# Kernel optimization log

Hardware: AMD Instinct MI355X
Metric: run time of the kernel (lower is better)

Reference implementation:

```python
import jax, jax.numpy as jnp
import numpy as np

N_NODES = 50000
N_REL = 8
D_IN = 128
D_OUT = 128
N_EDGES = 800000


def setup_inputs() -> dict:
    key = jax.random.key(0)
    k = jax.random.split(key, 6)
    # Xavier-ish scales for the learned params
    w_scale = (6.0 / (D_IN + D_OUT)) ** 0.5
    X = jax.random.normal(k[0], (N_NODES, D_IN), dtype=jnp.float32)
    W = jax.random.uniform(k[1], (N_REL, D_IN, D_OUT), dtype=jnp.float32,
                           minval=-w_scale, maxval=w_scale)
    W0 = jax.random.uniform(k[2], (D_IN, D_OUT), dtype=jnp.float32,
                            minval=-w_scale, maxval=w_scale)
    inv_norm = jnp.ones((N_REL, N_NODES), dtype=jnp.float32)  # init'd to ones in torch
    # COO edge list encoding the stacked sparse adjacency tensor adj_tensor[r, dst, src]
    edge_src = jax.random.randint(k[3], (N_EDGES,), 0, N_NODES, dtype=jnp.int32)
    edge_dst = jax.random.randint(k[4], (N_EDGES,), 0, N_NODES, dtype=jnp.int32)
    edge_rel = jax.random.randint(k[5], (N_EDGES,), 0, N_REL, dtype=jnp.int32)
    return {"X": X, "W": W, "W0": W0, "inv_norm": inv_norm,
            "edge_src": edge_src, "edge_dst": edge_dst, "edge_rel": edge_rel}


def reference(X, W, W0, inv_norm, edge_src, edge_dst, edge_rel) -> jnp.ndarray:
    # Per relation r:  inv_norm[r][:,None] * (A_r @ (X @ W[r]))  ; summed over r
    R, N = inv_norm.shape
    # Dense per-relation transform: [R, N, D_OUT]
    XW = jnp.einsum('nd,rde->rne', X, W)
    # Sparse A_r @ XW_r as gather over source nodes + scatter-add into (rel, dst)
    msgs = XW[edge_rel, edge_src]                       # [E, D_OUT]
    seg_ids = edge_rel * N + edge_dst                   # combined (rel, dst) segment id
    agg = jax.ops.segment_sum(msgs, seg_ids, num_segments=R * N)
    agg = agg.reshape(R, N, -1)                         # [R, N, D_OUT]
    incoming = jnp.sum(agg * inv_norm[:, :, None], axis=0)  # [N, D_OUT]
    self_connection = X @ W0
    return incoming + self_connection
```

## Files before the change

kernel.cpp:

```cpp
#include <hip/hip_runtime.h>

typedef __attribute__((ext_vector_type(8))) short short8;
typedef __attribute__((ext_vector_type(4))) float f32x4;

__device__ __forceinline__ unsigned short f2bf(float f) {
    unsigned u = __float_as_uint(f);
    u += 0x7FFF + ((u >> 16) & 1);
    return (unsigned short)(u >> 16);
}

__device__ __forceinline__ float readlane_f(float v, int l) {
    return __int_as_float(__builtin_amdgcn_readlane(__float_as_int(v), l));
}

__device__ __forceinline__ float bflo(unsigned u) { return __uint_as_float(u << 16); }
__device__ __forceinline__ float bfhi(unsigned u) { return __uint_as_float(u & 0xFFFF0000u); }

__global__ __launch_bounds__(256) void hist_kernel(
    const int* __restrict__ edst, const int* __restrict__ erel,
    int* __restrict__ counts, int E)
{
    int i = blockIdx.x * 256 + threadIdx.x;
    const int stride = gridDim.x * 256;
    for (; i < E; i += stride)
        atomicAdd(&counts[edst[i] * 8 + erel[i]], 1);
}

__global__ __launch_bounds__(256) void scan1_kernel(
    const int* __restrict__ counts, int* __restrict__ blockSums, int KB)
{
    __shared__ int sd[256];
    const int t = threadIdx.x;
    const int base = blockIdx.x * 1024 + t * 4;
    int s = 0;
#pragma unroll
    for (int i = 0; i < 4; ++i) { int idx = base + i; if (idx < KB) s += counts[idx]; }
    sd[t] = s; __syncthreads();
    for (int off = 128; off > 0; off >>= 1) {
        if (t < off) sd[t] += sd[t + off];
        __syncthreads();
    }
    if (t == 0) blockSums[blockIdx.x] = sd[0];
}

__global__ __launch_bounds__(512) void scan2_kernel(int* blockSums, int nb)
{
    __shared__ int sd[512];
    const int t = threadIdx.x;
    const int v = (t < nb) ? blockSums[t] : 0;
    sd[t] = v; __syncthreads();
    for (int off = 1; off < 512; off <<= 1) {
        int x = (t >= off) ? sd[t - off] : 0;
        __syncthreads();
        sd[t] += x;
        __syncthreads();
    }
    if (t < nb) blockSums[t] = sd[t] - v;
}

__global__ __launch_bounds__(256) void scan3_kernel(
    const int* __restrict__ counts, const int* __restrict__ blockSums,
    int* __restrict__ starts, int KB)
{
    __shared__ int sd[256];
    const int t = threadIdx.x;
    const int base = blockIdx.x * 1024 + t * 4;
    int c[4]; int s = 0;
#pragma unroll
    for (int i = 0; i < 4; ++i) { int idx = base + i; c[i] = (idx < KB) ? counts[idx] : 0; s += c[i]; }
    sd[t] = s; __syncthreads();
    for (int off = 1; off < 256; off <<= 1) {
        int x = (t >= off) ? sd[t - off] : 0;
        __syncthreads();
        sd[t] += x;
        __syncthreads();
    }
    int run = sd[t] - s + blockSums[blockIdx.x];
#pragma unroll
    for (int i = 0; i < 4; ++i) {
        int idx = base + i;
        if (idx < KB) starts[idx] = run;
        run += c[i];
    }
}

__global__ __launch_bounds__(256) void cursor_init_kernel(
    const int* __restrict__ starts, int* __restrict__ cursor, int C)
{
    const int b = blockIdx.x * 256 + threadIdx.x;
    if (b < C) cursor[b] = starts[(b << 8) * 8];
}

#define PART_EPB 2048
#define CMAX 8192
__global__ __launch_bounds__(256) void partition_kernel(
    const int* __restrict__ esrc, const int* __restrict__ edst,
    const int* __restrict__ erel, int* __restrict__ cursor,
    unsigned* __restrict__ staged, int E, int C)
{
    __shared__ int lh[CMAX];
    const int t = threadIdx.x;
    const int base = blockIdx.x * PART_EPB;
    const int end = min(base + PART_EPB, E);

    for (int i = t; i < C; i += 256) lh[i] = 0;
    __syncthreads();
    for (int i = base + t; i < end; i += 256)
        atomicAdd(&lh[edst[i] >> 8], 1);
    __syncthreads();
    for (int i = t; i < C; i += 256) {
        const int c = lh[i];
        lh[i] = c ? atomicAdd(&cursor[i], c) : 0;
    }
    __syncthreads();
    for (int i = base + t; i < end; i += 256) {
        const int d = edst[i];
        const int pos = atomicAdd(&lh[d >> 8], 1);
        staged[pos] = (unsigned)esrc[i] | ((unsigned)(d & 255) << 21)
                    | ((unsigned)erel[i] << 29);
    }
}

__global__ __launch_bounds__(256) void binsort_kernel(
    const unsigned* __restrict__ staged, const int* __restrict__ starts,
    unsigned* __restrict__ sorted, int N, int E)
{
    __shared__ int lcur[2048];
    const int b = blockIdx.x;
    const int t = threadIdx.x;
    const int d0 = b << 8;
    const int binBase = d0 * 8;
    const int dEnd = min(d0 + 256, N);
    const int nbins = (dEnd - d0) * 8;
    const int base = starts[binBase];
    const int end = (dEnd < N) ? starts[dEnd * 8] : E;

    for (int i = t; i < nbins; i += 256)
        lcur[i] = starts[binBase + i];
    __syncthreads();

    for (int i = base + t; i < end; i += 256) {
        const unsigned v = staged[i];
        const unsigned src = v & 0x1FFFFFu;
        const int dlow = (int)((v >> 21) & 255u);
        const unsigned rel = v >> 29;
        const int pos = atomicAdd(&lcur[dlow * 8 + (int)rel], 1);
        sorted[pos] = src | (rel << 28);
    }
}

__global__ __launch_bounds__(256) void cast_kernel(
    const float* __restrict__ X, const float* __restrict__ W,
    const float* __restrict__ W0, unsigned short* __restrict__ Xb,
    unsigned short* __restrict__ Bt, int M, int R)
{
    const int ktot = (R + 1) * 128;
    const int nx = M * 32;
    const int idx = blockIdx.x * 256 + threadIdx.x;
    if (idx < nx) {
        const float4 v = ((const float4*)X)[idx];
        uint2 p;
        p.x = (unsigned)f2bf(v.x) | ((unsigned)f2bf(v.y) << 16);
        p.y = (unsigned)f2bf(v.z) | ((unsigned)f2bf(v.w) << 16);
        *(uint2*)(Xb + (size_t)idx * 4) = p;
    } else if (idx < nx + 128 * ktot) {
        const int e = idx - nx;
        const int n = e / ktot;
        const int k = e - n * ktot;
        const float v = (k < R * 128) ? W[(size_t)k * 128 + n]
                                      : W0[(size_t)(k - R * 128) * 128 + n];
        Bt[(size_t)n * ktot + k] = f2bf(v);
    }
}

#define ACC(P, U) switch ((P) >> 28) {                                   \
        case 0: ax0 += bflo(U); ay0 += bfhi(U); break;                   \
        case 1: ax1 += bflo(U); ay1 += bfhi(U); break;                   \
        case 2: ax2 += bflo(U); ay2 += bfhi(U); break;                   \
        case 3: ax3 += bflo(U); ay3 += bfhi(U); break;                   \
        case 4: ax4 += bflo(U); ay4 += bfhi(U); break;                   \
        case 5: ax5 += bflo(U); ay5 += bfhi(U); break;                   \
        case 6: ax6 += bflo(U); ay6 += bfhi(U); break;                   \
        default: ax7 += bflo(U); ay7 += bfhi(U); break; }

__global__ __launch_bounds__(256) void aggregate_kernel(
    const unsigned short* __restrict__ Xb, const float* __restrict__ inv_norm,
    const unsigned* __restrict__ sorted, const int* __restrict__ starts,
    unsigned short* __restrict__ A, int N, int E)
{
    const int dst = (int)((blockIdx.x * blockDim.x + threadIdx.x) >> 6);
    if (dst >= N) return;
    const int lane = threadIdx.x & 63;

    const int start = starts[dst * 8];
    const int end = (dst + 1 < N) ? starts[dst * 8 + 8] : E;

    float ax0=0,ay0=0, ax1=0,ay1=0, ax2=0,ay2=0, ax3=0,ay3=0;
    float ax4=0,ay4=0, ax5=0,ay5=0, ax6=0,ay6=0, ax7=0,ay7=0;

    for (int cb = start; cb < end; cb += 64) {
        const int take = min(64, end - cb);
        unsigned batch = 0;
        if (cb + lane < end) batch = sorted[cb + lane];
        int j = 0;
        for (; j + 8 <= take; j += 8) {
            unsigned p[8], u[8];
#pragma unroll
            for (int q = 0; q < 8; ++q)
                p[q] = (unsigned)__builtin_amdgcn_readlane((int)batch, j + q);
#pragma unroll
            for (int q = 0; q < 8; ++q)
                u[q] = ((const unsigned*)(Xb + ((size_t)(p[q] & 0x0FFFFFFFu) << 7)))[lane];
            ACC(p[0], u[0]); ACC(p[1], u[1]); ACC(p[2], u[2]); ACC(p[3], u[3]);
            ACC(p[4], u[4]); ACC(p[5], u[5]); ACC(p[6], u[6]); ACC(p[7], u[7]);
        }
        for (; j + 4 <= take; j += 4) {
            const unsigned p0 = (unsigned)__builtin_amdgcn_readlane((int)batch, j);
            const unsigned p1 = (unsigned)__builtin_amdgcn_readlane((int)batch, j + 1);
            const unsigned p2 = (unsigned)__builtin_amdgcn_readlane((int)batch, j + 2);
            const unsigned p3 = (unsigned)__builtin_amdgcn_readlane((int)batch, j + 3);
            const unsigned u0 = ((const unsigned*)(Xb + ((size_t)(p0 & 0x0FFFFFFFu) << 7)))[lane];
            const unsigned u1 = ((const unsigned*)(Xb + ((size_t)(p1 & 0x0FFFFFFFu) << 7)))[lane];
            const unsigned u2 = ((const unsigned*)(Xb + ((size_t)(p2 & 0x0FFFFFFFu) << 7)))[lane];
            const unsigned u3 = ((const unsigned*)(Xb + ((size_t)(p3 & 0x0FFFFFFFu) << 7)))[lane];
            ACC(p0, u0); ACC(p1, u1); ACC(p2, u2); ACC(p3, u3);
        }
        for (; j < take; ++j) {
            const unsigned p = (unsigned)__builtin_amdgcn_readlane((int)batch, j);
            const unsigned u = ((const unsigned*)(Xb + ((size_t)(p & 0x0FFFFFFFu) << 7)))[lane];
            ACC(p, u);
        }
    }

    const float nv_l = (lane < 8) ? inv_norm[(size_t)lane * N + dst] : 0.f;

    unsigned short* Arow = A + (size_t)dst * 1024 + lane * 2;
    {
        float s;
        s = readlane_f(nv_l, 0); *(unsigned*)(Arow + 0*128) = (unsigned)f2bf(ax0*s) | ((unsigned)f2bf(ay0*s) << 16);
        s = readlane_f(nv_l, 1); *(unsigned*)(Arow + 1*128) = (unsigned)f2bf(ax1*s) | ((unsigned)f2bf(ay1*s) << 16);
        s = readlane_f(nv_l, 2); *(unsigned*)(Arow + 2*128) = (unsigned)f2bf(ax2*s) | ((unsigned)f2bf(ay2*s) << 16);
        s = readlane_f(nv_l, 3); *(unsigned*)(Arow + 3*128) = (unsigned)f2bf(ax3*s) | ((unsigned)f2bf(ay3*s) << 16);
        s = readlane_f(nv_l, 4); *(unsigned*)(Arow + 4*128) = (unsigned)f2bf(ax4*s) | ((unsigned)f2bf(ay4*s) << 16);
        s = readlane_f(nv_l, 5); *(unsigned*)(Arow + 5*128) = (unsigned)f2bf(ax5*s) | ((unsigned)f2bf(ay5*s) << 16);
        s = readlane_f(nv_l, 6); *(unsigned*)(Arow + 6*128) = (unsigned)f2bf(ax6*s) | ((unsigned)f2bf(ay6*s) << 16);
        s = readlane_f(nv_l, 7); *(unsigned*)(Arow + 7*128) = (unsigned)f2bf(ax7*s) | ((unsigned)f2bf(ay7*s) << 16);
    }
}

template <int KT>
__global__ __launch_bounds__(512) void gemm_kernel(
    const unsigned short* __restrict__ A, const unsigned short* __restrict__ Xb,
    const unsigned short* __restrict__ Bt, float* __restrict__ out, int M)
{
    constexpr int NI = KT / 64;
    constexpr int NA = (KT - 128) / 64;
    __shared__ unsigned short Asw[2][128 * 64];
    __shared__ unsigned short Bsw[2][128 * 64];

    const int tid = threadIdx.x;
    const int wave = tid >> 6;
    const int lane = tid & 63;
    const int ln = lane & 15, quad = lane >> 4;
    const int wm = wave & 3;
    const int wn = wave >> 2;
    const int m0 = blockIdx.x * 128;

    const int sr = tid >> 2;
    const int sq = tid & 3;
    int am = m0 + sr; if (am >= M) am = M - 1;
    const unsigned short* Ag = A  + (size_t)am * (KT - 128) + sq * 16;
    const unsigned short* Xg = Xb + (size_t)am * 128 + sq * 16;
    const unsigned short* Bg = Bt + (size_t)sr * KT + sq * 16;

    const int wofs0 = sr * 64 + ((((sq << 1) + 0) ^ (sr & 7)) << 3);
    const int wofs1 = sr * 64 + ((((sq << 1) + 1) ^ (sr & 7)) << 3);

    f32x4 acc[8] = {};
    short8 ra0, ra1, rb0, rb1;

    auto load_regs = [&](int ko) {
        const unsigned short* as = (ko < NA) ? (Ag + ko * 64) : (Xg + (ko - NA) * 64);
        ra0 = *(const short8*)(as);
        ra1 = *(const short8*)(as + 8);
        const unsigned short* bs = Bg + ko * 64;
        rb0 = *(const short8*)(bs);
        rb1 = *(const short8*)(bs + 8);
    };
    auto write_lds = [&](int buf) {
        *(short8*)&Asw[buf][wofs0] = ra0;
        *(short8*)&Asw[buf][wofs1] = ra1;
        *(short8*)&Bsw[buf][wofs0] = rb0;
        *(short8*)&Bsw[buf][wofs1] = rb1;
    };

    load_regs(0);
    write_lds(0);
    __syncthreads();

    int cur = 0;
#pragma unroll
    for (int ko = 0; ko < NI; ++ko) {
        if (ko + 1 < NI) load_regs(ko + 1);
        __builtin_amdgcn_sched_barrier(0);
#pragma unroll
        for (int ks = 0; ks < 2; ++ks) {
            short8 af[2], bf[4];
#pragma unroll
            for (int mi = 0; mi < 2; ++mi) {
                const int r = wm * 32 + mi * 16 + ln;
                af[mi] = *(const short8*)&Asw[cur][r * 64 + ((((ks << 2) + quad) ^ (r & 7)) << 3)];
            }
#pragma unroll
            for (int ci = 0; ci < 4; ++ci) {
                const int r = wn * 64 + ci * 16 + ln;
                bf[ci] = *(const short8*)&Bsw[cur][r * 64 + ((((ks << 2) + quad) ^ (r & 7)) << 3)];
            }
#pragma unroll
            for (int mi = 0; mi < 2; ++mi)
#pragma unroll
                for (int ci = 0; ci < 4; ++ci)
                    acc[mi * 4 + ci] = __builtin_amdgcn_mfma_f32_16x16x32_bf16(
                        af[mi], bf[ci], acc[mi * 4 + ci], 0, 0, 0);
        }
        __builtin_amdgcn_sched_barrier(0);
        if (ko + 1 < NI) write_lds(cur ^ 1);
        __syncthreads();
        cur ^= 1;
    }

#pragma unroll
    for (int mi = 0; mi < 2; ++mi)
#pragma unroll
        for (int ci = 0; ci < 4; ++ci)
#pragma unroll
            for (int rg = 0; rg < 4; ++rg) {
                const int row = m0 + wm * 32 + mi * 16 + quad * 4 + rg;
                if (row < M)
                    out[(size_t)row * 128 + wn * 64 + ci * 16 + ln] = acc[mi * 4 + ci][rg];
            }
}

__global__ __launch_bounds__(256) void gemm_kernel_rt(
    const unsigned short* __restrict__ A, const unsigned short* __restrict__ Xb,
    const unsigned short* __restrict__ Bt, float* __restrict__ out,
    int M, int ktot)
{
    const int tid = threadIdx.x;
    const int wave = tid >> 6;
    const int lane = tid & 63;
    const int ln = lane & 15, quad = lane >> 4;
    const int m0 = blockIdx.x * 64 + wave * 16;
    int m = m0 + ln; if (m >= M) m = M - 1;
    const unsigned short* Arow = A + (size_t)m * (ktot - 128) + quad * 8;
    const unsigned short* Xrow = Xb + (size_t)m * 128 + quad * 8;
    const unsigned short* Bbase = Bt + (size_t)ln * ktot + quad * 8;

    f32x4 acc[8] = {};
    for (int kb = 0; kb < (ktot >> 5); ++kb) {
        const int k0 = kb << 5;
        const unsigned short* asrc = (k0 < ktot - 128) ? (Arow + k0) : (Xrow + (k0 - (ktot - 128)));
        const short8 a = *(const short8*)asrc;
#pragma unroll
        for (int c = 0; c < 8; ++c) {
            const short8 b = *(const short8*)(Bbase + (size_t)c * 16 * ktot + k0);
            acc[c] = __builtin_amdgcn_mfma_f32_16x16x32_bf16(a, b, acc[c], 0, 0, 0);
        }
    }
#pragma unroll
    for (int c = 0; c < 8; ++c) {
#pragma unroll
        for (int rg = 0; rg < 4; ++rg) {
            const int row = m0 + quad * 4 + rg;
            if (row < M) out[(size_t)row * 128 + c * 16 + ln] = acc[c][rg];
        }
    }
}

extern "C" void kernel_launch(void* const* d_in, const int* in_sizes, int n_in,
                              void* d_out, int out_size, void* d_ws, size_t ws_size,
                              hipStream_t stream) {
    const float* X        = (const float*)d_in[0];
    const float* W        = (const float*)d_in[1];
    const float* W0       = (const float*)d_in[2];
    const float* inv_norm = (const float*)d_in[3];
    const int*   esrc     = (const int*)d_in[4];
    const int*   edst     = (const int*)d_in[5];
    const int*   erel     = (const int*)d_in[6];
    float* out = (float*)d_out;

    const int N  = in_sizes[0] / 128;
    const int E  = in_sizes[4];
    const int R  = in_sizes[3] / N;
    const int KB = N * 8;
    const int ktot = (R + 1) * 128;
    const int C  = (N + 255) >> 8;

    char* ws = (char*)d_ws;
    size_t off = 0;
    auto alloc = [&](size_t bytes) -> char* {
        char* p = ws + off; off = (off + bytes + 255) & ~(size_t)255; return p;
    };
    unsigned short* A         = (unsigned short*)alloc((size_t)N * R * 128 * 2);
    unsigned short* Xb        = (unsigned short*)alloc((size_t)N * 128 * 2);
    unsigned short* Bt        = (unsigned short*)alloc((size_t)128 * ktot * 2);
    int*            counts    = (int*)alloc((size_t)KB * 4);
    int*            starts    = (int*)alloc((size_t)KB * 4);
    int*            blockSums = (int*)alloc(512 * 4);
    int*            cursor    = (int*)alloc((size_t)C * 4);
    unsigned*       staged    = (unsigned*)alloc((size_t)E * 4);
    unsigned*       sorted    = (unsigned*)alloc((size_t)E * 4);
    (void)ws_size;

    const int nScanBlocks = (KB + 1023) / 1024;
    const int nPartBlocks = (E + PART_EPB - 1) / PART_EPB;

    hipMemsetAsync(counts, 0, (size_t)KB * 4, stream);
    hist_kernel<<<2048, 256, 0, stream>>>(edst, erel, counts, E);
    scan1_kernel<<<nScanBlocks, 256, 0, stream>>>(counts, blockSums, KB);
    scan2_kernel<<<1, 512, 0, stream>>>(blockSums, nScanBlocks);
    scan3_kernel<<<nScanBlocks, 256, 0, stream>>>(counts, blockSums, starts, KB);
    cursor_init_kernel<<<(C + 255) / 256, 256, 0, stream>>>(starts, cursor, C);
    partition_kernel<<<nPartBlocks, 256, 0, stream>>>(esrc, edst, erel, cursor, staged, E, C);
    binsort_kernel<<<C, 256, 0, stream>>>(staged, starts, sorted, N, E);
    cast_kernel<<<(N * 32 + 128 * ktot + 255) / 256, 256, 0, stream>>>(X, W, W0, Xb, Bt, N, R);
    aggregate_kernel<<<(N + 3) / 4, 256, 0, stream>>>(Xb, inv_norm, sorted, starts, A, N, E);
    if (ktot == 1152)
        gemm_kernel<1152><<<(N + 127) / 128, 512, 0, stream>>>(A, Xb, Bt, out, N);
    else
        gemm_kernel_rt<<<(N + 63) / 64, 256, 0, stream>>>(A, Xb, Bt, out, N, ktot);
}
```

Before: 231.1 us.

## Fuse edge aggregation and GEMM into one kernel staging aggregates in LDS

The separate aggregate and GEMM kernels are replaced by one fused kernel for the default 1152-wide case. Each 64-row block aggregates messages for four relations at a time into swizzled shared memory, then runs MFMA over those slices with B read straight from global memory, and finishes with the self-connection from X. This removes the round trip of the large bf16 aggregate matrix A through HBM and one launch. In exchange the block runs gather and MFMA phases serially with barriers in between, B is re-read from global memory without LDS reuse, and the 64 KB of shared memory per block may limit occupancy.

```diff
diff --git a/kernel.cpp b/kernel.cpp
--- a/kernel.cpp
+++ b/kernel.cpp
@@ -173,6 +173,158 @@
     }
 }
 
+#define ACC4(P, U) switch (((P) >> 28) & 3) {                            \
+        case 0: bx0 += bflo(U); by0 += bfhi(U); break;                   \
+        case 1: bx1 += bflo(U); by1 += bfhi(U); break;                   \
+        case 2: bx2 += bflo(U); by2 += bfhi(U); break;                   \
+        default: bx3 += bflo(U); by3 += bfhi(U); break; }
+
+template <int KT>
+__global__ __launch_bounds__(512) void fused_kernel(
+    const unsigned short* __restrict__ Xb, const float* __restrict__ inv_norm,
+    const unsigned* __restrict__ sorted, const int* __restrict__ starts,
+    const unsigned short* __restrict__ Bt, float* __restrict__ out,
+    int N, int E)
+{
+    __shared__ unsigned short Sg[4 * 64 * 128];
+
+    const int tid = threadIdx.x;
+    const int wave = tid >> 6, lane = tid & 63;
+    const int ln = lane & 15, quad = lane >> 4;
+    const int wm = wave & 3, wn = wave >> 2;
+    const int m0 = blockIdx.x * 64;
+    const int KB = N * 8;
+
+    const int wr_chunk = lane >> 2;
+    const int wr_within = (lane & 3) << 1;
+
+    f32x4 acc[4] = {};
+
+    auto phaseA = [&](int r0) {
+#pragma unroll 1
+        for (int i = 0; i < 8; ++i) {
+            const int dl = (wave << 3) + i;
+            const int d = m0 + dl;
+            float bx0=0,by0=0, bx1=0,by1=0, bx2=0,by2=0, bx3=0,by3=0;
+            if (d < N) {
+                const int bs = starts[d * 8 + r0];
+                const int ei = d * 8 + r0 + 4;
+                const int be = (ei < KB) ? starts[ei] : E;
+                for (int cb = bs; cb < be; cb += 64) {
+                    const int take = min(64, be - cb);
+                    unsigned batch = 0;
+                    if (cb + lane < be) batch = sorted[cb + lane];
+                    int j = 0;
+                    for (; j + 8 <= take; j += 8) {
+                        unsigned p[8], u[8];
+#pragma unroll
+                        for (int q = 0; q < 8; ++q)
+                            p[q] = (unsigned)__builtin_amdgcn_readlane((int)batch, j + q);
+#pragma unroll
+                        for (int q = 0; q < 8; ++q)
+                            u[q] = ((const unsigned*)(Xb + ((size_t)(p[q] & 0x0FFFFFFFu) << 7)))[lane];
+                        ACC4(p[0], u[0]); ACC4(p[1], u[1]); ACC4(p[2], u[2]); ACC4(p[3], u[3]);
+                        ACC4(p[4], u[4]); ACC4(p[5], u[5]); ACC4(p[6], u[6]); ACC4(p[7], u[7]);
+                    }
+                    for (; j + 4 <= take; j += 4) {
+                        const unsigned p0 = (unsigned)__builtin_amdgcn_readlane((int)batch, j);
+                        const unsigned p1 = (unsigned)__builtin_amdgcn_readlane((int)batch, j + 1);
+                        const unsigned p2 = (unsigned)__builtin_amdgcn_readlane((int)batch, j + 2);
+                        const unsigned p3 = (unsigned)__builtin_amdgcn_readlane((int)batch, j + 3);
+                        const unsigned u0 = ((const unsigned*)(Xb + ((size_t)(p0 & 0x0FFFFFFFu) << 7)))[lane];
+                        const unsigned u1 = ((const unsigned*)(Xb + ((size_t)(p1 & 0x0FFFFFFFu) << 7)))[lane];
+                        const unsigned u2 = ((const unsigned*)(Xb + ((size_t)(p2 & 0x0FFFFFFFu) << 7)))[lane];
+                        const unsigned u3 = ((const unsigned*)(Xb + ((size_t)(p3 & 0x0FFFFFFFu) << 7)))[lane];
+                        ACC4(p0, u0); ACC4(p1, u1); ACC4(p2, u2); ACC4(p3, u3);
+                    }
+                    for (; j < take; ++j) {
+                        const unsigned p = (unsigned)__builtin_amdgcn_readlane((int)batch, j);
+                        const unsigned u = ((const unsigned*)(Xb + ((size_t)(p & 0x0FFFFFFFu) << 7)))[lane];
+                        ACC4(p, u);
+                    }
+                }
+            }
+            const int dd = min(d, N - 1);
+            {
+                const float s = inv_norm[(size_t)(r0 + 0) * N + dd];
+                const unsigned w = (unsigned)f2bf(bx0 * s) | ((unsigned)f2bf(by0 * s) << 16);
+                const int row = 0 * 64 + dl;
+                *(unsigned*)&Sg[row * 128 + (((wr_chunk ^ (row & 7)) << 3)) + wr_within] = w;
+            }
+            {
+                const float s = inv_norm[(size_t)(r0 + 1) * N + dd];
+                const unsigned w = (unsigned)f2bf(bx1 * s) | ((unsigned)f2bf(by1 * s) << 16);
+                const int row = 1 * 64 + dl;
+                *(unsigned*)&Sg[row * 128 + (((wr_chunk ^ (row & 7)) << 3)) + wr_within] = w;
+            }
+            {
+                const float s = inv_norm[(size_t)(r0 + 2) * N + dd];
+                const unsigned w = (unsigned)f2bf(bx2 * s) | ((unsigned)f2bf(by2 * s) << 16);
+                const int row = 2 * 64 + dl;
+                *(unsigned*)&Sg[row * 128 + (((wr_chunk ^ (row & 7)) << 3)) + wr_within] = w;
+            }
+            {
+                const float s = inv_norm[(size_t)(r0 + 3) * N + dd];
+                const unsigned w = (unsigned)f2bf(bx3 * s) | ((unsigned)f2bf(by3 * s) << 16);
+                const int row = 3 * 64 + dl;
+                *(unsigned*)&Sg[row * 128 + (((wr_chunk ^ (row & 7)) << 3)) + wr_within] = w;
+            }
+        }
+    };
+
+    auto phaseX = [&]() {
+#pragma unroll 1
+        for (int i = 0; i < 8; ++i) {
+            const int dl = (wave << 3) + i;
+            const int dd = min(m0 + dl, N - 1);
+            const unsigned u = ((const unsigned*)(Xb + ((size_t)dd << 7)))[lane];
+            const int row = dl;
+            *(unsigned*)&Sg[row * 128 + (((wr_chunk ^ (row & 7)) << 3)) + wr_within] = u;
+        }
+    };
+
+    auto phaseB = [&](int rglob, int rg) {
+        const int srow = rg * 64 + wm * 16 + ln;
+        const int sbase = srow * 128;
+        const int sx = srow & 7;
+#pragma unroll
+        for (int ks = 0; ks < 4; ++ks) {
+            const short8 a = *(const short8*)&Sg[sbase + ((((ks << 2) + quad) ^ sx) << 3)];
+#pragma unroll
+            for (int nf = 0; nf < 4; ++nf) {
+                const int n = wn * 64 + nf * 16 + ln;
+                const short8 b = *(const short8*)&Bt[(size_t)n * KT + rglob * 128 + (ks << 5) + (quad << 3)];
+                acc[nf] = __builtin_amdgcn_mfma_f32_16x16x32_bf16(a, b, acc[nf], 0, 0, 0);
+            }
+        }
+    };
+
+    phaseA(0);
+    __syncthreads();
+#pragma unroll
+    for (int rg = 0; rg < 4; ++rg) phaseB(rg, rg);
+    __syncthreads();
+
+    phaseA(4);
+    __syncthreads();
+#pragma unroll
+    for (int rg = 0; rg < 4; ++rg) phaseB(4 + rg, rg);
+    __syncthreads();
+
+    phaseX();
+    __syncthreads();
+    phaseB(8, 0);
+
+#pragma unroll
+    for (int nf = 0; nf < 4; ++nf)
+#pragma unroll
+        for (int rg = 0; rg < 4; ++rg) {
+            const int row = m0 + wm * 16 + quad * 4 + rg;
+            if (row < N)
+                out[(size_t)row * 128 + wn * 64 + nf * 16 + ln] = acc[nf][rg];
+        }
+}
+
 #define ACC(P, U) switch ((P) >> 28) {                                   \
         case 0: ax0 += bflo(U); ay0 += bfhi(U); break;                   \
         case 1: ax1 += bflo(U); ay1 += bfhi(U); break;                   \
@@ -202,30 +354,7 @@
         const int take = min(64, end - cb);
         unsigned batch = 0;
         if (cb + lane < end) batch = sorted[cb + lane];
-        int j = 0;
-        for (; j + 8 <= take; j += 8) {
-            unsigned p[8], u[8];
-#pragma unroll
-            for (int q = 0; q < 8; ++q)
-                p[q] = (unsigned)__builtin_amdgcn_readlane((int)batch, j + q);
-#pragma unroll
-            for (int q = 0; q < 8; ++q)
-                u[q] = ((const unsigned*)(Xb + ((size_t)(p[q] & 0x0FFFFFFFu) << 7)))[lane];
-            ACC(p[0], u[0]); ACC(p[1], u[1]); ACC(p[2], u[2]); ACC(p[3], u[3]);
-            ACC(p[4], u[4]); ACC(p[5], u[5]); ACC(p[6], u[6]); ACC(p[7], u[7]);
-        }
-        for (; j + 4 <= take; j += 4) {
-            const unsigned p0 = (unsigned)__builtin_amdgcn_readlane((int)batch, j);
-            const unsigned p1 = (unsigned)__builtin_amdgcn_readlane((int)batch, j + 1);
-            const unsigned p2 = (unsigned)__builtin_amdgcn_readlane((int)batch, j + 2);
-            const unsigned p3 = (unsigned)__builtin_amdgcn_readlane((int)batch, j + 3);
-            const unsigned u0 = ((const unsigned*)(Xb + ((size_t)(p0 & 0x0FFFFFFFu) << 7)))[lane];
-            const unsigned u1 = ((const unsigned*)(Xb + ((size_t)(p1 & 0x0FFFFFFFu) << 7)))[lane];
-            const unsigned u2 = ((const unsigned*)(Xb + ((size_t)(p2 & 0x0FFFFFFFu) << 7)))[lane];
-            const unsigned u3 = ((const unsigned*)(Xb + ((size_t)(p3 & 0x0FFFFFFFu) << 7)))[lane];
-            ACC(p0, u0); ACC(p1, u1); ACC(p2, u2); ACC(p3, u3);
-        }
-        for (; j < take; ++j) {
+        for (int j = 0; j < take; ++j) {
             const unsigned p = (unsigned)__builtin_amdgcn_readlane((int)batch, j);
             const unsigned u = ((const unsigned*)(Xb + ((size_t)(p & 0x0FFFFFFFu) << 7)))[lane];
             ACC(p, u);
@@ -233,7 +362,6 @@
     }
 
     const float nv_l = (lane < 8) ? inv_norm[(size_t)lane * N + dst] : 0.f;
-
     unsigned short* Arow = A + (size_t)dst * 1024 + lane * 2;
     {
         float s;
@@ -246,99 +374,6 @@
         s = readlane_f(nv_l, 6); *(unsigned*)(Arow + 6*128) = (unsigned)f2bf(ax6*s) | ((unsigned)f2bf(ay6*s) << 16);
         s = readlane_f(nv_l, 7); *(unsigned*)(Arow + 7*128) = (unsigned)f2bf(ax7*s) | ((unsigned)f2bf(ay7*s) << 16);
     }
-}
-
-template <int KT>
-__global__ __launch_bounds__(512) void gemm_kernel(
-    const unsigned short* __restrict__ A, const unsigned short* __restrict__ Xb,
-    const unsigned short* __restrict__ Bt, float* __restrict__ out, int M)
-{
-    constexpr int NI = KT / 64;
-    constexpr int NA = (KT - 128) / 64;
-    __shared__ unsigned short Asw[2][128 * 64];
-    __shared__ unsigned short Bsw[2][128 * 64];
-
-    const int tid = threadIdx.x;
-    const int wave = tid >> 6;
-    const int lane = tid & 63;
-    const int ln = lane & 15, quad = lane >> 4;
-    const int wm = wave & 3;
-    const int wn = wave >> 2;
-    const int m0 = blockIdx.x * 128;
-
-    const int sr = tid >> 2;
-    const int sq = tid & 3;
-    int am = m0 + sr; if (am >= M) am = M - 1;
-    const unsigned short* Ag = A  + (size_t)am * (KT - 128) + sq * 16;
-    const unsigned short* Xg = Xb + (size_t)am * 128 + sq * 16;
-    const unsigned short* Bg = Bt + (size_t)sr * KT + sq * 16;
-
-    const int wofs0 = sr * 64 + ((((sq << 1) + 0) ^ (sr & 7)) << 3);
-    const int wofs1 = sr * 64 + ((((sq << 1) + 1) ^ (sr & 7)) << 3);
-
-    f32x4 acc[8] = {};
-    short8 ra0, ra1, rb0, rb1;
-
-    auto load_regs = [&](int ko) {
-        const unsigned short* as = (ko < NA) ? (Ag + ko * 64) : (Xg + (ko - NA) * 64);
-        ra0 = *(const short8*)(as);
-        ra1 = *(const short8*)(as + 8);
-        const unsigned short* bs = Bg + ko * 64;
-        rb0 = *(const short8*)(bs);
-        rb1 = *(const short8*)(bs + 8);
-    };
-    auto write_lds = [&](int buf) {
-        *(short8*)&Asw[buf][wofs0] = ra0;
-        *(short8*)&Asw[buf][wofs1] = ra1;
-        *(short8*)&Bsw[buf][wofs0] = rb0;
-        *(short8*)&Bsw[buf][wofs1] = rb1;
-    };
-
-    load_regs(0);
-    write_lds(0);
-    __syncthreads();
-
-    int cur = 0;
-#pragma unroll
-    for (int ko = 0; ko < NI; ++ko) {
-        if (ko + 1 < NI) load_regs(ko + 1);
-        __builtin_amdgcn_sched_barrier(0);
-#pragma unroll
-        for (int ks = 0; ks < 2; ++ks) {
-            short8 af[2], bf[4];
-#pragma unroll
-            for (int mi = 0; mi < 2; ++mi) {
-                const int r = wm * 32 + mi * 16 + ln;
-                af[mi] = *(const short8*)&Asw[cur][r * 64 + ((((ks << 2) + quad) ^ (r & 7)) << 3)];
-            }
-#pragma unroll
-            for (int ci = 0; ci < 4; ++ci) {
-                const int r = wn * 64 + ci * 16 + ln;
-                bf[ci] = *(const short8*)&Bsw[cur][r * 64 + ((((ks << 2) + quad) ^ (r & 7)) << 3)];
-            }
-#pragma unroll
-            for (int mi = 0; mi < 2; ++mi)
-#pragma unroll
-                for (int ci = 0; ci < 4; ++ci)
-                    acc[mi * 4 + ci] = __builtin_amdgcn_mfma_f32_16x16x32_bf16(
-                        af[mi], bf[ci], acc[mi * 4 + ci], 0, 0, 0);
-        }
-        __builtin_amdgcn_sched_barrier(0);
-        if (ko + 1 < NI) write_lds(cur ^ 1);
-        __syncthreads();
-        cur ^= 1;
-    }
-
-#pragma unroll
-    for (int mi = 0; mi < 2; ++mi)
-#pragma unroll
-        for (int ci = 0; ci < 4; ++ci)
-#pragma unroll
-            for (int rg = 0; rg < 4; ++rg) {
-                const int row = m0 + wm * 32 + mi * 16 + quad * 4 + rg;
-                if (row < M)
-                    out[(size_t)row * 128 + wn * 64 + ci * 16 + ln] = acc[mi * 4 + ci][rg];
-            }
 }
 
 __global__ __launch_bounds__(256) void gemm_kernel_rt(
@@ -424,9 +459,11 @@
     partition_kernel<<<nPartBlocks, 256, 0, stream>>>(esrc, edst, erel, cursor, staged, E, C);
     binsort_kernel<<<C, 256, 0, stream>>>(staged, starts, sorted, N, E);
     cast_kernel<<<(N * 32 + 128 * ktot + 255) / 256, 256, 0, stream>>>(X, W, W0, Xb, Bt, N, R);
-    aggregate_kernel<<<(N + 3) / 4, 256, 0, stream>>>(Xb, inv_norm, sorted, starts, A, N, E);
-    if (ktot == 1152)
-        gemm_kernel<1152><<<(N + 127) / 128, 512, 0, stream>>>(A, Xb, Bt, out, N);
-    else
+    if (ktot == 1152) {
+        fused_kernel<1152><<<(N + 63) / 64, 512, 0, stream>>>(
+            Xb, inv_norm, sorted, starts, Bt, out, N, E);
+    } else {
+        aggregate_kernel<<<(N + 3) / 4, 256, 0, stream>>>(Xb, inv_norm, sorted, starts, A, N, E);
         gemm_kernel_rt<<<(N + 63) / 64, 256, 0, stream>>>(A, Xb, Bt, out, N, ktot);
-}
+    }
+}
```

New measurement: 366.5 us. 58.6% more time.

## Replace fine-grained global histogram and scan with coarse chunk histogram plus in-block scan

Applied to the files above, without the earlier changes.

Removes the per-(dst,rel) global atomic histogram and the three-kernel multi-block scan. Edges are now counted per 256-node chunk with shared-memory atomics, and a single-block kernel scans those counts and writes both chunk starts and partition cursors. The fine per-bin starts are computed inside binsort with a local histogram and block scan. This cuts kernel launches and global atomic traffic, at the cost of binsort reading the staged edges twice and both chist and cscan assuming at most 2048 chunks.

```diff
diff --git a/kernel.cpp b/kernel.cpp
--- a/kernel.cpp
+++ b/kernel.cpp
@@ -16,58 +16,37 @@
 __device__ __forceinline__ float bflo(unsigned u) { return __uint_as_float(u << 16); }
 __device__ __forceinline__ float bfhi(unsigned u) { return __uint_as_float(u & 0xFFFF0000u); }
 
-__global__ __launch_bounds__(256) void hist_kernel(
-    const int* __restrict__ edst, const int* __restrict__ erel,
-    int* __restrict__ counts, int E)
-{
-    int i = blockIdx.x * 256 + threadIdx.x;
-    const int stride = gridDim.x * 256;
-    for (; i < E; i += stride)
-        atomicAdd(&counts[edst[i] * 8 + erel[i]], 1);
-}
-
-__global__ __launch_bounds__(256) void scan1_kernel(
-    const int* __restrict__ counts, int* __restrict__ blockSums, int KB)
+#define CHB 2048
+__global__ __launch_bounds__(256) void chist_kernel(
+    const int* __restrict__ edst, int* __restrict__ ccounts, int E, int C)
+{
+    __shared__ int lh[CHB];
+    const int t = threadIdx.x;
+    for (int i = t; i < C; i += 256) lh[i] = 0;
+    __syncthreads();
+    const int base = blockIdx.x * 2048;
+    const int end = min(base + 2048, E);
+    for (int i = base + t; i < end; i += 256)
+        atomicAdd(&lh[edst[i] >> 8], 1);
+    __syncthreads();
+    for (int i = t; i < C; i += 256)
+        if (lh[i]) atomicAdd(&ccounts[i], lh[i]);
+}
+
+__global__ __launch_bounds__(256) void cscan_kernel(
+    const int* __restrict__ ccounts, int* __restrict__ cstarts,
+    int* __restrict__ cursor, int C)
 {
     __shared__ int sd[256];
     const int t = threadIdx.x;
-    const int base = blockIdx.x * 1024 + t * 4;
-    int s = 0;
-#pragma unroll
-    for (int i = 0; i < 4; ++i) { int idx = base + i; if (idx < KB) s += counts[idx]; }
-    sd[t] = s; __syncthreads();
-    for (int off = 128; off > 0; off >>= 1) {
-        if (t < off) sd[t] += sd[t + off];
-        __syncthreads();
-    }
-    if (t == 0) blockSums[blockIdx.x] = sd[0];
-}
-
-__global__ __launch_bounds__(512) void scan2_kernel(int* blockSums, int nb)
-{
-    __shared__ int sd[512];
-    const int t = threadIdx.x;
-    const int v = (t < nb) ? blockSums[t] : 0;
-    sd[t] = v; __syncthreads();
-    for (int off = 1; off < 512; off <<= 1) {
-        int x = (t >= off) ? sd[t - off] : 0;
-        __syncthreads();
-        sd[t] += x;
-        __syncthreads();
-    }
-    if (t < nb) blockSums[t] = sd[t] - v;
-}
-
-__global__ __launch_bounds__(256) void scan3_kernel(
-    const int* __restrict__ counts, const int* __restrict__ blockSums,
-    int* __restrict__ starts, int KB)
-{
-    __shared__ int sd[256];
-    const int t = threadIdx.x;
-    const int base = blockIdx.x * 1024 + t * 4;
-    int c[4]; int s = 0;
-#pragma unroll
-    for (int i = 0; i < 4; ++i) { int idx = base + i; c[i] = (idx < KB) ? counts[idx] : 0; s += c[i]; }
+    const int per = (C + 255) >> 8;
+    int c[8]; int s = 0;
+#pragma unroll
+    for (int k = 0; k < 8; ++k) {
+        const int idx = t * per + k;
+        c[k] = (k < per && idx < C) ? ccounts[idx] : 0;
+        s += c[k];
+    }
     sd[t] = s; __syncthreads();
     for (int off = 1; off < 256; off <<= 1) {
         int x = (t >= off) ? sd[t - off] : 0;
@@ -75,30 +54,22 @@
         sd[t] += x;
         __syncthreads();
     }
-    int run = sd[t] - s + blockSums[blockIdx.x];
-#pragma unroll
-    for (int i = 0; i < 4; ++i) {
-        int idx = base + i;
-        if (idx < KB) starts[idx] = run;
-        run += c[i];
-    }
-}
-
-__global__ __launch_bounds__(256) void cursor_init_kernel(
-    const int* __restrict__ starts, int* __restrict__ cursor, int C)
-{
-    const int b = blockIdx.x * 256 + threadIdx.x;
-    if (b < C) cursor[b] = starts[(b << 8) * 8];
+    int run = sd[t] - s;
+#pragma unroll
+    for (int k = 0; k < 8; ++k) {
+        const int idx = t * per + k;
+        if (k < per && idx < C) { cstarts[idx] = run; cursor[idx] = run; }
+        run += c[k];
+    }
 }
 
 #define PART_EPB 2048
-#define CMAX 8192
 __global__ __launch_bounds__(256) void partition_kernel(
     const int* __restrict__ esrc, const int* __restrict__ edst,
     const int* __restrict__ erel, int* __restrict__ cursor,
     unsigned* __restrict__ staged, int E, int C)
 {
-    __shared__ int lh[CMAX];
+    __shared__ int lh[CHB];
     const int t = threadIdx.x;
     const int base = blockIdx.x * PART_EPB;
     const int end = min(base + PART_EPB, E);
@@ -122,29 +93,51 @@
 }
 
 __global__ __launch_bounds__(256) void binsort_kernel(
-    const unsigned* __restrict__ staged, const int* __restrict__ starts,
-    unsigned* __restrict__ sorted, int N, int E)
+    const unsigned* __restrict__ staged, const int* __restrict__ cstarts,
+    int* __restrict__ starts, unsigned* __restrict__ sorted,
+    int N, int E, int C)
 {
     __shared__ int lcur[2048];
+    __shared__ int wsum[256];
     const int b = blockIdx.x;
     const int t = threadIdx.x;
     const int d0 = b << 8;
     const int binBase = d0 * 8;
-    const int dEnd = min(d0 + 256, N);
-    const int nbins = (dEnd - d0) * 8;
-    const int base = starts[binBase];
-    const int end = (dEnd < N) ? starts[dEnd * 8] : E;
-
-    for (int i = t; i < nbins; i += 256)
-        lcur[i] = starts[binBase + i];
-    __syncthreads();
-
+    const int nbins = (min(d0 + 256, N) - d0) * 8;
+    const int base = cstarts[b];
+    const int end = (b + 1 < C) ? cstarts[b + 1] : E;
+
+    for (int i = t; i < 2048; i += 256) lcur[i] = 0;
+    __syncthreads();
+    for (int i = base + t; i < end; i += 256) {
+        const unsigned v = staged[i];
+        atomicAdd(&lcur[(int)((v >> 21) & 255u) * 8 + (int)(v >> 29)], 1);
+    }
+    __syncthreads();
+    const int b8 = t * 8;
+    int c[8]; int s = 0;
+#pragma unroll
+    for (int k = 0; k < 8; ++k) { c[k] = lcur[b8 + k]; s += c[k]; }
+    wsum[t] = s; __syncthreads();
+    for (int off = 1; off < 256; off <<= 1) {
+        int x = (t >= off) ? wsum[t - off] : 0;
+        __syncthreads();
+        wsum[t] += x;
+        __syncthreads();
+    }
+    int run = wsum[t] - s + base;
+#pragma unroll
+    for (int k = 0; k < 8; ++k) {
+        lcur[b8 + k] = run;
+        if (b8 + k < nbins) starts[binBase + b8 + k] = run;
+        run += c[k];
+    }
+    __syncthreads();
     for (int i = base + t; i < end; i += 256) {
         const unsigned v = staged[i];
         const unsigned src = v & 0x1FFFFFu;
-        const int dlow = (int)((v >> 21) & 255u);
         const unsigned rel = v >> 29;
-        const int pos = atomicAdd(&lcur[dlow * 8 + (int)rel], 1);
+        const int pos = atomicAdd(&lcur[(int)((v >> 21) & 255u) * 8 + (int)rel], 1);
         sorted[pos] = src | (rel << 28);
     }
 }
@@ -404,25 +397,21 @@
     unsigned short* A         = (unsigned short*)alloc((size_t)N * R * 128 * 2);
     unsigned short* Xb        = (unsigned short*)alloc((size_t)N * 128 * 2);
     unsigned short* Bt        = (unsigned short*)alloc((size_t)128 * ktot * 2);
-    int*            counts    = (int*)alloc((size_t)KB * 4);
+    int*            ccounts   = (int*)alloc((size_t)C * 4);
+    int*            cstarts   = (int*)alloc((size_t)C * 4);
+    int*            cursor    = (int*)alloc((size_t)C * 4);
     int*            starts    = (int*)alloc((size_t)KB * 4);
-    int*            blockSums = (int*)alloc(512 * 4);
-    int*            cursor    = (int*)alloc((size_t)C * 4);
     unsigned*       staged    = (unsigned*)alloc((size_t)E * 4);
     unsigned*       sorted    = (unsigned*)alloc((size_t)E * 4);
     (void)ws_size;
 
-    const int nScanBlocks = (KB + 1023) / 1024;
-    const int nPartBlocks = (E + PART_EPB - 1) / PART_EPB;
-
-    hipMemsetAsync(counts, 0, (size_t)KB * 4, stream);
-    hist_kernel<<<2048, 256, 0, stream>>>(edst, erel, counts, E);
-    scan1_kernel<<<nScanBlocks, 256, 0, stream>>>(counts, blockSums, KB);
-    scan2_kernel<<<1, 512, 0, stream>>>(blockSums, nScanBlocks);
-    scan3_kernel<<<nScanBlocks, 256, 0, stream>>>(counts, blockSums, starts, KB);
-    cursor_init_kernel<<<(C + 255) / 256, 256, 0, stream>>>(starts, cursor, C);
-    partition_kernel<<<nPartBlocks, 256, 0, stream>>>(esrc, edst, erel, cursor, staged, E, C);
-    binsort_kernel<<<C, 256, 0, stream>>>(staged, starts, sorted, N, E);
+    const int nEdgeBlocks = (E + 2047) / 2048;
+
+    hipMemsetAsync(ccounts, 0, (size_t)C * 4, stream);
+    chist_kernel<<<nEdgeBlocks, 256, 0, stream>>>(edst, ccounts, E, C);
+    cscan_kernel<<<1, 256, 0, stream>>>(ccounts, cstarts, cursor, C);
+    partition_kernel<<<nEdgeBlocks, 256, 0, stream>>>(esrc, edst, erel, cursor, staged, E, C);
+    binsort_kernel<<<C, 256, 0, stream>>>(staged, cstarts, starts, sorted, N, E, C);
     cast_kernel<<<(N * 32 + 128 * ktot + 255) / 256, 256, 0, stream>>>(X, W, W0, Xb, Bt, N, R);
     aggregate_kernel<<<(N + 3) / 4, 256, 0, stream>>>(Xb, inv_norm, sorted, starts, A, N, E);
     if (ktot == 1152)
```

After: 207.3 us. -10.3%, faster.
